# Performance work log

Measured on AMD Instinct MI355X. Metric: run time of the kernel, lower is better.

Reference implementation:

```python
import jax, jax.numpy as jnp
import numpy as np

B, S, E = 2, 2048, 2048
H, G = 16, 4
HD = E // H  # 128 head dim


def setup_inputs() -> dict:
    key = jax.random.key(0)
    k1, k2, k3, k4 = jax.random.split(key, 4)
    x = jax.random.normal(k1, (B, S, E), dtype=jnp.float32)
    mask = jnp.zeros((B, 1, S, S), dtype=jnp.float32)
    # torch nn.Linear weights stored as [in, out] for x @ W
    W1 = jax.random.normal(k2, (E, 2 * G * HD), dtype=jnp.float32) * 0.02
    W2 = jax.random.normal(k3, (E, E), dtype=jnp.float32) * 0.02
    W3 = jax.random.normal(k4, (E, E), dtype=jnp.float32) * 0.02
    return {"x": x, "mask": mask, "W1": W1, "W2": W2, "W3": W3}


def reference(x, mask, W1, W2, W3):
    b, s, e_model = x.shape
    hd = e_model // H
    # linear_1 -> rearrange 'b s (n g e) -> n b g s e'
    kv = (x @ W1).reshape(b, s, 2, G, hd).transpose(2, 0, 3, 1, 4)
    k, v = kv[0], kv[1]  # [b, g, s, e]
    # linear_2 -> 'b t (h e) -> b h t e'
    q = (x @ W2).reshape(b, s, H, hd).transpose(0, 2, 1, 3)  # [b, h, t, e]
    # NOTE: g is summed out here, exactly as in the source einsum (no sqrt scaling)
    score = jnp.einsum('bhte,bgse->bhts', q, k)
    score = jax.nn.softmax(score + mask, axis=-1)
    out = jnp.einsum('bhts,bgse->bthe', score, v)  # g summed again
    out = out.reshape(b, s, e_model)
    return out @ W3
```

## Files before the change

### kernel.cpp

```cpp
#include <hip/hip_runtime.h>
#include <cstdint>

#define S_LEN 2048
#define EMB   2048
#define NHEAD 16
#define HDIM  128
#define NFUSE 2304
#define LOG2E 1.4426950408889634f

typedef __attribute__((ext_vector_type(8))) _Float16 h8;
typedef __attribute__((ext_vector_type(4))) _Float16 h4;
typedef __attribute__((ext_vector_type(8))) short short8;
typedef __attribute__((ext_vector_type(4))) short short4v;
typedef __attribute__((ext_vector_type(4))) float f32x4;
typedef unsigned int u32;

__device__ inline short f2bf(float x) {
  union { float f; uint32_t u; } v; v.f = x;
  uint32_t r = v.u + 0x7fffu + ((v.u >> 16) & 1u);
  return (short)(r >> 16);
}
__device__ inline float bf2f(short b) {
  union { uint32_t u; float f; } v; v.u = ((uint32_t)(uint16_t)b) << 16;
  return v.f;
}
__device__ inline float fexp2(float x) {
  float r;
  __asm__ volatile("v_exp_f32 %0, %1" : "=v"(r) : "v"(x));
  return r;
}
__device__ inline u32 pkrtz(float a, float b) {
  u32 r;
  __asm__ volatile("v_cvt_pkrtz_f16_f32 %0, %1, %2" : "=v"(r) : "v"(a), "v"(b));
  return r;
}
__device__ inline void glds16(const void* g, void* l) {
  __builtin_amdgcn_global_load_lds(
      (const __attribute__((address_space(1))) u32*)g,
      (__attribute__((address_space(3))) u32*)l, 16, 0, 0);
}

__global__ __launch_bounds__(256) void reduce_w1_kernel(
    const float* __restrict__ W1, float* __restrict__ Wkv) {
  int idx = blockIdx.x * 256 + threadIdx.x;
  int i = idx >> 8;
  int c = idx & 255;
  int base = (c < 128) ? c : (c + 384);
  const float* r = W1 + (size_t)i * 1024 + base;
  Wkv[idx] = (r[0] + r[128]) + (r[256] + r[384]);
}

__global__ __launch_bounds__(256) void cvt_x_kernel(
    const float* __restrict__ src, _Float16* __restrict__ dst) {
  size_t idx = (size_t)blockIdx.x * 256 + threadIdx.x;
  float4 v = *(const float4*)(src + idx * 4);
  h4 o;
  o[0] = (_Float16)v.x; o[1] = (_Float16)v.y;
  o[2] = (_Float16)v.z; o[3] = (_Float16)v.w;
  *(h4*)(dst + idx * 4) = o;
}

__global__ __launch_bounds__(256) void cvt_mask_kernel(
    const float* __restrict__ src, short* __restrict__ dst) {
  size_t idx = (size_t)blockIdx.x * 256 + threadIdx.x;
  float4 v = *(const float4*)(src + idx * 4);
  short4v o;
  o[0] = f2bf(v.x * LOG2E); o[1] = f2bf(v.y * LOG2E);
  o[2] = f2bf(v.z * LOG2E); o[3] = f2bf(v.w * LOG2E);
  *(short4v*)(dst + idx * 4) = o;
}

__global__ __launch_bounds__(256) void transpose_f16_kernel(
    const float* __restrict__ W, _Float16* __restrict__ T, int K, int N) {
  __shared__ float Tt[64][65];
  const int tid = threadIdx.x;
  const int k0 = blockIdx.y * 64, n0 = blockIdx.x * 64;
  {
    int r = tid >> 2, c0 = (tid & 3) * 16;
    const float* src = W + (size_t)(k0 + r) * N + n0 + c0;
#pragma unroll
    for (int j = 0; j < 4; ++j) {
      float4 v = *(const float4*)(src + 4 * j);
      Tt[r][c0 + 4 * j + 0] = v.x; Tt[r][c0 + 4 * j + 1] = v.y;
      Tt[r][c0 + 4 * j + 2] = v.z; Tt[r][c0 + 4 * j + 3] = v.w;
    }
  }
  __syncthreads();
  {
    int n = tid >> 2, kc = (tid & 3) * 16;
    h8 o0, o1;
#pragma unroll
    for (int i = 0; i < 8; ++i) {
      o0[i] = (_Float16)Tt[kc + i][n];
      o1[i] = (_Float16)Tt[kc + 8 + i][n];
    }
    size_t off = (size_t)(n0 + n) * K + k0 + kc;
    *(h8*)(T + off) = o0;
    *(h8*)(T + off + 8) = o1;
  }
}

template <bool QSCALE>
__global__ __launch_bounds__(256, 3) void gemm_f16(
    const _Float16* __restrict__ A, const _Float16* __restrict__ Bt,
    float* __restrict__ C, _Float16* __restrict__ Cf,
    int M, int N, int K, int qlim) {
  extern __shared__ char smraw[];
  _Float16* sm = (_Float16*)smraw;
  const int BUFS = 8192;

  const int tid  = threadIdx.x;
  const int w    = tid >> 6;
  const int lane = tid & 63;
  const int quad = lane >> 4, col16 = lane & 15;
  const int row0 = blockIdx.y * 128, col0 = blockIdx.x * 128;
  const float esc = (col0 < qlim) ? LOG2E : 1.0f;

  const int srow  = w * 32 + (lane >> 2);
  const int kpart = (lane & 3) * 8;
  const _Float16* pA0 = A + (size_t)(row0 + srow) * K + kpart;
  const _Float16* pA1 = pA0 + (size_t)16 * K;
  const _Float16* pB0 = Bt + (size_t)(col0 + srow) * K + kpart;
  const _Float16* pB1 = pB0 + (size_t)16 * K;

  const int oA0 = (w * 32) * 32, oA1 = (w * 32 + 16) * 32;
  const int oB0 = 4096 + (w * 32) * 32, oB1 = 4096 + (w * 32 + 16) * 32;

#define STAGE_GEMM(bo)                                                        \
  do {                                                                        \
    glds16(pA0, sm + (bo) + oA0); glds16(pA1, sm + (bo) + oA1);               \
    glds16(pB0, sm + (bo) + oB0); glds16(pB1, sm + (bo) + oB1);               \
    pA0 += 32; pA1 += 32; pB0 += 32; pB1 += 32;                               \
  } while (0)

  f32x4 acc[2][8];
#pragma unroll
  for (int mt = 0; mt < 2; ++mt)
#pragma unroll
    for (int nt = 0; nt < 8; ++nt) {
      acc[mt][nt][0] = 0.f; acc[mt][nt][1] = 0.f;
      acc[mt][nt][2] = 0.f; acc[mt][nt][3] = 0.f;
    }

  const int nchunk = K >> 5;
  int bo = 0;
  STAGE_GEMM(0);

#pragma unroll 1
  for (int c = 0; c < nchunk; ++c) {
    if (c + 1 < nchunk) {
      STAGE_GEMM(bo ^ BUFS);
      __asm__ volatile("s_waitcnt vmcnt(4)" ::: "memory");
    } else {
      __asm__ volatile("s_waitcnt vmcnt(0)" ::: "memory");
    }
    __builtin_amdgcn_s_barrier();

    const _Float16* AS = sm + bo;
    const _Float16* BS = sm + bo + 4096;

    h8 af[2];
#pragma unroll
    for (int mt = 0; mt < 2; ++mt)
      af[mt] = *(const h8*)&AS[(w * 32 + mt * 16 + col16) * 32 + quad * 8];
#pragma unroll
    for (int nt = 0; nt < 8; ++nt) {
      h8 b8 = *(const h8*)&BS[(nt * 16 + col16) * 32 + quad * 8];
#pragma unroll
      for (int mt = 0; mt < 2; ++mt)
        acc[mt][nt] = __builtin_amdgcn_mfma_f32_16x16x32_f16(af[mt], b8, acc[mt][nt], 0, 0, 0);
    }
    __builtin_amdgcn_s_barrier();
    bo ^= BUFS;
  }
#undef STAGE_GEMM

#pragma unroll
  for (int mt = 0; mt < 2; ++mt)
#pragma unroll
    for (int nt = 0; nt < 8; ++nt)
#pragma unroll
      for (int r = 0; r < 4; ++r) {
        int row = row0 + w * 32 + mt * 16 + quad * 4 + r;
        int col = col0 + nt * 16 + col16;
        float v = acc[mt][nt][r];
        if constexpr (QSCALE) {
          Cf[(size_t)row * N + col] = (_Float16)(v * esc);
        } else {
          C[(size_t)row * N + col] = v;
        }
      }
}

__global__ __launch_bounds__(256) void build_vt(
    const short* __restrict__ QKh, short* __restrict__ VT) {
  __shared__ short T[64][136];
  const int tid = threadIdx.x;
  const int gs = blockIdx.x * 64;
  const int b = gs >> 11;
  const int s = gs & 2047;
  {
    int r = tid >> 2, c0 = (tid & 3) * 32;
    const short* src = QKh + (size_t)(gs + r) * NFUSE + 2176 + c0;
#pragma unroll
    for (int j = 0; j < 4; ++j)
      *(short8*)&T[r][c0 + 8 * j] = *(const short8*)(src + 8 * j);
  }
  __syncthreads();
  {
    int d = tid >> 1, c = (tid & 1) * 32;
    short* dst = VT + (size_t)(b * HDIM + d) * S_LEN + s + c;
#pragma unroll
    for (int jo = 0; jo < 4; ++jo) {
      short8 o;
#pragma unroll
      for (int i = 0; i < 8; ++i) o[i] = T[c + jo * 8 + i][d];
      *(short8*)(dst + jo * 8) = o;
    }
  }
}

__global__ __launch_bounds__(256, 2) void flash_f16(
    const _Float16* __restrict__ QKf, const _Float16* __restrict__ VT,
    const short* __restrict__ maskb, _Float16* __restrict__ AO) {
  __shared__ _Float16 KS[64 * 128];
  __shared__ _Float16 VtS[128 * 64];
  __shared__ _Float16 PsS[2 * 4 * 16 * 64];

  const int tid   = threadIdx.x;
  const int w     = tid >> 6;
  const int lane  = tid & 63;
  const int quad  = lane >> 4;
  const int col16 = lane & 15;
  const int xq    = col16 & 7;
  const int bh = blockIdx.y, b = bh >> 4, h = bh & 15;
  const int t0 = blockIdx.x * 128;

  const int jr = lane >> 4;
  const int kg = lane & 15;
  const int vr = lane >> 3;
  const int vg = lane & 7;

  _Float16* myK = KS + w * 2048;
  _Float16* myV = VtS + w * 2048;

  h8 qf[2][4];
#pragma unroll
  for (int t = 0; t < 2; ++t) {
#pragma unroll
    for (int j = 0; j < 4; ++j) {
      int rl = 4 * j + jr;
      int gq = kg ^ (rl & 7);
      size_t go = (size_t)(b * S_LEN + t0 + 64 * t + 16 * w + rl) * NFUSE
                + h * HDIM + gq * 8;
      glds16(QKf + go, myK + j * 512);
    }
    __asm__ volatile("s_waitcnt vmcnt(0)" ::: "memory");
#pragma unroll
    for (int c = 0; c < 4; ++c)
      qf[t][c] = *(const h8*)&myK[col16 * 128 + (((c * 4 + quad) ^ xq) * 8)];
    __asm__ volatile("s_waitcnt lgkmcnt(0)" ::: "memory");
  }

  const _Float16* Kbase = QKf + (size_t)b * S_LEN * NFUSE + 2048;
  const _Float16* Vbase = VT + (size_t)b * HDIM * S_LEN;
  u32 offK[4], offV[4];
#pragma unroll
  for (int j = 0; j < 4; ++j) {
    int rl = 4 * j + jr;
    offK[j] = (u32)(16 * w + rl) * NFUSE + (u32)((kg ^ (rl & 7)) * 8);
    int dl = 32 * w + 8 * j + vr;
    offV[j] = (u32)dl * S_LEN + (u32)((vg ^ (vr & 7)) * 8);
  }
  const short* pM[2];
#pragma unroll
  for (int t = 0; t < 2; ++t)
    pM[t] = maskb + (size_t)b * S_LEN * S_LEN
          + (size_t)(t0 + 64 * t + 16 * w + col16) * S_LEN + quad * 4;

#pragma unroll
  for (int j = 0; j < 4; ++j) glds16(Kbase + offK[j], myK + j * 512);
#pragma unroll
  for (int j = 0; j < 4; ++j) glds16(Vbase + offV[j], myV + j * 512);
#pragma unroll
  for (int j = 0; j < 4; ++j) { offK[j] += 64 * NFUSE; offV[j] += 64; }

  f32x4 oacc[2][8];
#pragma unroll
  for (int t = 0; t < 2; ++t)
#pragma unroll
    for (int d = 0; d < 8; ++d) {
      oacc[t][d][0] = 0.f; oacc[t][d][1] = 0.f;
      oacc[t][d][2] = 0.f; oacc[t][d][3] = 0.f;
    }
  float mrow[2] = {-3.0e38f, -3.0e38f};
  float lrow[2] = {0.f, 0.f};

#pragma unroll 1
  for (int it = 0; it < S_LEN / 64; ++it) {
    __asm__ volatile("s_waitcnt vmcnt(4)" ::: "memory");
    __builtin_amdgcn_s_barrier();

    short4v msk[2][4];
#pragma unroll
    for (int t = 0; t < 2; ++t)
#pragma unroll
      for (int nt = 0; nt < 4; ++nt)
        msk[t][nt] = *(const short4v*)(pM[t] + nt * 16);

    f32x4 sacc[2][4];
#pragma unroll
    for (int t = 0; t < 2; ++t)
#pragma unroll
      for (int nt = 0; nt < 4; ++nt) {
        sacc[t][nt][0] = 0.f; sacc[t][nt][1] = 0.f;
        sacc[t][nt][2] = 0.f; sacc[t][nt][3] = 0.f;
      }
    __builtin_amdgcn_s_setprio(1);
#pragma unroll
    for (int c = 0; c < 4; ++c)
#pragma unroll
      for (int nt = 0; nt < 4; ++nt) {
        h8 k8 = *(const h8*)&KS[(nt * 16 + col16) * 128 + (((c * 4 + quad) ^ xq) * 8)];
#pragma unroll
        for (int t = 0; t < 2; ++t)
          sacc[t][nt] = __builtin_amdgcn_mfma_f32_16x16x32_f16(k8, qf[t][c], sacc[t][nt], 0, 0, 0);
      }
    __builtin_amdgcn_s_setprio(0);

    __asm__ volatile("s_waitcnt lgkmcnt(0)" ::: "memory");
    __builtin_amdgcn_s_barrier();
    if (it + 1 < S_LEN / 64) {
#pragma unroll
      for (int j = 0; j < 4; ++j) glds16(Kbase + offK[j], myK + j * 512);
#pragma unroll
      for (int j = 0; j < 4; ++j) offK[j] += 64 * NFUSE;
    }

    if (it + 1 < S_LEN / 64) {
      __asm__ volatile("s_waitcnt vmcnt(4)" ::: "memory");
    } else {
      __asm__ volatile("s_waitcnt vmcnt(0)" ::: "memory");
    }

#pragma unroll
    for (int t = 0; t < 2; ++t) {
      float vv[4][4];
#pragma unroll
      for (int nt = 0; nt < 4; ++nt)
#pragma unroll
        for (int r = 0; r < 4; ++r)
          vv[nt][r] = sacc[t][nt][r] + bf2f(msk[t][nt][r]);
      float mx = vv[0][0];
#pragma unroll
      for (int nt = 0; nt < 4; ++nt)
#pragma unroll
        for (int r = 0; r < 4; ++r) mx = fmaxf(mx, vv[nt][r]);
      mx = fmaxf(mx, __shfl_xor(mx, 16));
      mx = fmaxf(mx, __shfl_xor(mx, 32));

      float nm = fmaxf(mrow[t], mx);
      if (__all(mx - mrow[t] <= 8.0f)) {
        nm = mrow[t];
      } else {
        float al = fexp2(mrow[t] - nm);
        lrow[t] *= al;
#pragma unroll
        for (int d = 0; d < 8; ++d) {
          oacc[t][d][0] *= al; oacc[t][d][1] *= al;
          oacc[t][d][2] *= al; oacc[t][d][3] *= al;
        }
        mrow[t] = nm;
      }

      float ps = 0.f;
      u32 pk0[4], pk1[4];
#pragma unroll
      for (int nt = 0; nt < 4; ++nt) {
        float p0 = fexp2(vv[nt][0] - nm);
        float p1 = fexp2(vv[nt][1] - nm);
        float p2 = fexp2(vv[nt][2] - nm);
        float p3 = fexp2(vv[nt][3] - nm);
        ps += (p0 + p1) + (p2 + p3);
        pk0[nt] = pkrtz(p0, p1);
        pk1[nt] = pkrtz(p2, p3);
      }
      ps += __shfl_xor(ps, 16);
      ps += __shfl_xor(ps, 32);
      lrow[t] += ps;

      int pbase = ((t * 4 + w) * 16 + col16) * 64 + (quad & 1) * 4;
#pragma unroll
      for (int nt = 0; nt < 4; ++nt) {
        uint2 pv2; pv2.x = pk0[nt]; pv2.y = pk1[nt];
        *(uint2*)&PsS[pbase + (((2 * nt + (quad >> 1)) ^ xq) * 8)] = pv2;
      }
    }

    __asm__ volatile("s_waitcnt lgkmcnt(0)" ::: "memory");
    h8 pa[2][2];
#pragma unroll
    for (int t = 0; t < 2; ++t) {
      int pb = ((t * 4 + w) * 16 + col16) * 64;
      pa[t][0] = *(const h8*)&PsS[pb + ((quad ^ xq) * 8)];
      pa[t][1] = *(const h8*)&PsS[pb + (((4 + quad) ^ xq) * 8)];
    }
    __builtin_amdgcn_s_setprio(1);
#pragma unroll
    for (int d = 0; d < 8; ++d) {
      int vo = (d * 16 + col16) * 64;
      h8 vb0 = *(const h8*)&VtS[vo + ((quad ^ xq) * 8)];
      h8 vb1 = *(const h8*)&VtS[vo + (((4 + quad) ^ xq) * 8)];
#pragma unroll
      for (int t = 0; t < 2; ++t) {
        oacc[t][d] = __builtin_amdgcn_mfma_f32_16x16x32_f16(vb0, pa[t][0], oacc[t][d], 0, 0, 0);
        oacc[t][d] = __builtin_amdgcn_mfma_f32_16x16x32_f16(vb1, pa[t][1], oacc[t][d], 0, 0, 0);
      }
    }
    __builtin_amdgcn_s_setprio(0);

    __asm__ volatile("s_waitcnt lgkmcnt(0)" ::: "memory");
    __builtin_amdgcn_s_barrier();
    if (it + 1 < S_LEN / 64) {
#pragma unroll
      for (int j = 0; j < 4; ++j) glds16(Vbase + offV[j], myV + j * 512);
#pragma unroll
      for (int j = 0; j < 4; ++j) offV[j] += 64;
    }
#pragma unroll
    for (int t = 0; t < 2; ++t) pM[t] += 64;
  }

#pragma unroll
  for (int t = 0; t < 2; ++t) {
    float inv = 1.0f / lrow[t];
    int q = t0 + 64 * t + 16 * w + col16;
    _Float16* dst = AO + (size_t)(b * S_LEN + q) * EMB + h * HDIM + quad * 4;
#pragma unroll
    for (int d = 0; d < 8; ++d) {
      h4 o4;
#pragma unroll
      for (int r = 0; r < 4; ++r) o4[r] = (_Float16)(oacc[t][d][r] * inv);
      *(h4*)(dst + d * 16) = o4;
    }
  }
}

extern "C" void kernel_launch(void* const* d_in, const int* in_sizes, int n_in,
                              void* d_out, int out_size, void* d_ws, size_t ws_size,
                              hipStream_t stream) {
  const float* x    = (const float*)d_in[0];
  const float* mask = (const float*)d_in[1];
  const float* W1   = (const float*)d_in[2];
  const float* W2   = (const float*)d_in[3];
  const float* W3   = (const float*)d_in[4];
  float* out = (float*)d_out;

  char* ws = (char*)d_ws;
  size_t off = 0;
  _Float16* xf   = (_Float16*)(ws + off); off += (size_t)4096 * 2048 * 2;
  _Float16* Wtf  = (_Float16*)(ws + off); off += (size_t)NFUSE * 2048 * 2;
  _Float16* QKf  = (_Float16*)(ws + off); off += (size_t)4096 * NFUSE * 2;
  _Float16* VT   = (_Float16*)(ws + off); off += (size_t)2 * 128 * 2048 * 2;
  _Float16* AOf  = (_Float16*)(ws + off); off += (size_t)4096 * 2048 * 2;
  float*    Wkv  = (float*)(ws + off);    off += (size_t)2048 * 256 * 4;
  short*    maskb= (short*)(ws + off);    off += (size_t)2 * 2048 * 2048 * 2;
  _Float16* W3t  = xf;

  reduce_w1_kernel<<<2048, 256, 0, stream>>>(W1, Wkv);
  cvt_x_kernel<<<8192, 256, 0, stream>>>(x, xf);
  cvt_mask_kernel<<<8192, 256, 0, stream>>>(mask, maskb);
  transpose_f16_kernel<<<dim3(32, 32), 256, 0, stream>>>(W2, Wtf, 2048, 2048);
  transpose_f16_kernel<<<dim3(4, 32), 256, 0, stream>>>(
      Wkv, Wtf + (size_t)2048 * 2048, 2048, 256);

  gemm_f16<true><<<dim3(NFUSE / 128, 32), 256, 32768, stream>>>(
      xf, Wtf, nullptr, QKf, 4096, NFUSE, 2048, 2048);

  build_vt<<<64, 256, 0, stream>>>((const short*)QKf, (short*)VT);

  flash_f16<<<dim3(S_LEN / 128, 2 * NHEAD), 256, 0, stream>>>(
      QKf, VT, maskb, AOf);

  transpose_f16_kernel<<<dim3(32, 32), 256, 0, stream>>>(W3, W3t, 2048, 2048);
  gemm_f16<false><<<dim3(16, 32), 256, 32768, stream>>>(
      AOf, W3t, out, nullptr, 4096, 2048, 2048, 0);
}
```

Measured before the change: 370.2 us.

## Halve flash query tile to 64 rows and stage mask tiles via LDS async loads

The flash attention kernel now processes 64 query rows per block instead of 128, which doubles the grid and halves per-thread accumulator registers. The mask is no longer read with direct global loads each iteration. It is prefetched into LDS with async global-to-LDS copies alongside K, and the wait counts are adjusted to match. This trades twice the K/V traffic per query and lower K/V reuse for higher occupancy and latency hiding, and takes mask loads off the critical path.

```diff
diff --git a/kernel.cpp b/kernel.cpp
--- a/kernel.cpp
+++ b/kernel.cpp
@@ -225,7 +225,8 @@
     const short* __restrict__ maskb, _Float16* __restrict__ AO) {
   __shared__ _Float16 KS[64 * 128];
   __shared__ _Float16 VtS[128 * 64];
-  __shared__ _Float16 PsS[2 * 4 * 16 * 64];
+  __shared__ _Float16 PsS[4 * 16 * 64];
+  __shared__ short    MkS[4 * 16 * 64];
 
   const int tid   = threadIdx.x;
   const int w     = tid >> 6;
@@ -234,7 +235,7 @@
   const int col16 = lane & 15;
   const int xq    = col16 & 7;
   const int bh = blockIdx.y, b = bh >> 4, h = bh & 15;
-  const int t0 = blockIdx.x * 128;
+  const int t0 = blockIdx.x * 64;
 
   const int jr = lane >> 4;
   const int kg = lane & 15;
@@ -243,28 +244,30 @@
 
   _Float16* myK = KS + w * 2048;
   _Float16* myV = VtS + w * 2048;
-
-  h8 qf[2][4];
-#pragma unroll
-  for (int t = 0; t < 2; ++t) {
+  short*    myM = MkS + w * 1024;
+  _Float16* myP = PsS + w * 1024;
+
+  h8 qf[4];
+  {
 #pragma unroll
     for (int j = 0; j < 4; ++j) {
       int rl = 4 * j + jr;
       int gq = kg ^ (rl & 7);
-      size_t go = (size_t)(b * S_LEN + t0 + 64 * t + 16 * w + rl) * NFUSE
+      size_t go = (size_t)(b * S_LEN + t0 + 16 * w + rl) * NFUSE
                 + h * HDIM + gq * 8;
       glds16(QKf + go, myK + j * 512);
     }
     __asm__ volatile("s_waitcnt vmcnt(0)" ::: "memory");
 #pragma unroll
     for (int c = 0; c < 4; ++c)
-      qf[t][c] = *(const h8*)&myK[col16 * 128 + (((c * 4 + quad) ^ xq) * 8)];
+      qf[c] = *(const h8*)&myK[col16 * 128 + (((c * 4 + quad) ^ xq) * 8)];
     __asm__ volatile("s_waitcnt lgkmcnt(0)" ::: "memory");
   }
 
   const _Float16* Kbase = QKf + (size_t)b * S_LEN * NFUSE + 2048;
   const _Float16* Vbase = VT + (size_t)b * HDIM * S_LEN;
-  u32 offK[4], offV[4];
+  const short*    Mbase = maskb + (size_t)b * S_LEN * S_LEN;
+  u32 offK[4], offV[4], offM[2];
 #pragma unroll
   for (int j = 0; j < 4; ++j) {
     int rl = 4 * j + jr;
@@ -272,59 +275,56 @@
     int dl = 32 * w + 8 * j + vr;
     offV[j] = (u32)dl * S_LEN + (u32)((vg ^ (vr & 7)) * 8);
   }
-  const short* pM[2];
-#pragma unroll
-  for (int t = 0; t < 2; ++t)
-    pM[t] = maskb + (size_t)b * S_LEN * S_LEN
-          + (size_t)(t0 + 64 * t + 16 * w + col16) * S_LEN + quad * 4;
+#pragma unroll
+  for (int j = 0; j < 2; ++j) {
+    int mrw = j * 8 + vr;
+    int mq  = t0 + 16 * w + mrw;
+    offM[j] = (u32)mq * S_LEN + (u32)((vg ^ (mrw & 7)) * 8);
+  }
 
 #pragma unroll
   for (int j = 0; j < 4; ++j) glds16(Kbase + offK[j], myK + j * 512);
 #pragma unroll
+  for (int j = 0; j < 2; ++j) glds16(Mbase + offM[j], myM + j * 512);
+#pragma unroll
   for (int j = 0; j < 4; ++j) glds16(Vbase + offV[j], myV + j * 512);
 #pragma unroll
   for (int j = 0; j < 4; ++j) { offK[j] += 64 * NFUSE; offV[j] += 64; }
-
-  f32x4 oacc[2][8];
-#pragma unroll
-  for (int t = 0; t < 2; ++t)
-#pragma unroll
-    for (int d = 0; d < 8; ++d) {
-      oacc[t][d][0] = 0.f; oacc[t][d][1] = 0.f;
-      oacc[t][d][2] = 0.f; oacc[t][d][3] = 0.f;
-    }
-  float mrow[2] = {-3.0e38f, -3.0e38f};
-  float lrow[2] = {0.f, 0.f};
+#pragma unroll
+  for (int j = 0; j < 2; ++j) offM[j] += 64;
+
+  f32x4 oacc[8];
+#pragma unroll
+  for (int d = 0; d < 8; ++d) {
+    oacc[d][0] = 0.f; oacc[d][1] = 0.f;
+    oacc[d][2] = 0.f; oacc[d][3] = 0.f;
+  }
+  float mrow = -3.0e38f, lrow = 0.f;
 
 #pragma unroll 1
   for (int it = 0; it < S_LEN / 64; ++it) {
     __asm__ volatile("s_waitcnt vmcnt(4)" ::: "memory");
     __builtin_amdgcn_s_barrier();
 
-    short4v msk[2][4];
-#pragma unroll
-    for (int t = 0; t < 2; ++t)
-#pragma unroll
-      for (int nt = 0; nt < 4; ++nt)
-        msk[t][nt] = *(const short4v*)(pM[t] + nt * 16);
-
-    f32x4 sacc[2][4];
-#pragma unroll
-    for (int t = 0; t < 2; ++t)
-#pragma unroll
-      for (int nt = 0; nt < 4; ++nt) {
-        sacc[t][nt][0] = 0.f; sacc[t][nt][1] = 0.f;
-        sacc[t][nt][2] = 0.f; sacc[t][nt][3] = 0.f;
-      }
+    short4v msk[4];
+#pragma unroll
+    for (int nt = 0; nt < 4; ++nt)
+      msk[nt] = *(const short4v*)
+          &myM[col16 * 64 + (((quad + nt * 4) ^ (xq << 1)) << 2)];
+
+    f32x4 sacc[4];
+#pragma unroll
+    for (int nt = 0; nt < 4; ++nt) {
+      sacc[nt][0] = 0.f; sacc[nt][1] = 0.f;
+      sacc[nt][2] = 0.f; sacc[nt][3] = 0.f;
+    }
     __builtin_amdgcn_s_setprio(1);
 #pragma unroll
     for (int c = 0; c < 4; ++c)
 #pragma unroll
       for (int nt = 0; nt < 4; ++nt) {
         h8 k8 = *(const h8*)&KS[(nt * 16 + col16) * 128 + (((c * 4 + quad) ^ xq) * 8)];
-#pragma unroll
-        for (int t = 0; t < 2; ++t)
-          sacc[t][nt] = __builtin_amdgcn_mfma_f32_16x16x32_f16(k8, qf[t][c], sacc[t][nt], 0, 0, 0);
+        sacc[nt] = __builtin_amdgcn_mfma_f32_16x16x32_f16(k8, qf[c], sacc[nt], 0, 0, 0);
       }
     __builtin_amdgcn_s_setprio(0);
 
@@ -334,23 +334,26 @@
 #pragma unroll
       for (int j = 0; j < 4; ++j) glds16(Kbase + offK[j], myK + j * 512);
 #pragma unroll
+      for (int j = 0; j < 2; ++j) glds16(Mbase + offM[j], myM + j * 512);
+#pragma unroll
       for (int j = 0; j < 4; ++j) offK[j] += 64 * NFUSE;
+#pragma unroll
+      for (int j = 0; j < 2; ++j) offM[j] += 64;
     }
 
     if (it + 1 < S_LEN / 64) {
-      __asm__ volatile("s_waitcnt vmcnt(4)" ::: "memory");
+      __asm__ volatile("s_waitcnt vmcnt(6)" ::: "memory");
     } else {
       __asm__ volatile("s_waitcnt vmcnt(0)" ::: "memory");
     }
 
-#pragma unroll
-    for (int t = 0; t < 2; ++t) {
+    {
       float vv[4][4];
 #pragma unroll
       for (int nt = 0; nt < 4; ++nt)
 #pragma unroll
         for (int r = 0; r < 4; ++r)
-          vv[nt][r] = sacc[t][nt][r] + bf2f(msk[t][nt][r]);
+          vv[nt][r] = sacc[nt][r] + bf2f(msk[nt][r]);
       float mx = vv[0][0];
 #pragma unroll
       for (int nt = 0; nt < 4; ++nt)
@@ -359,18 +362,18 @@
       mx = fmaxf(mx, __shfl_xor(mx, 16));
       mx = fmaxf(mx, __shfl_xor(mx, 32));
 
-      float nm = fmaxf(mrow[t], mx);
-      if (__all(mx - mrow[t] <= 8.0f)) {
-        nm = mrow[t];
+      float nm = fmaxf(mrow, mx);
+      if (__all(mx - mrow <= 8.0f)) {
+        nm = mrow;
       } else {
-        float al = fexp2(mrow[t] - nm);
-        lrow[t] *= al;
+        float al = fexp2(mrow - nm);
+        lrow *= al;
 #pragma unroll
         for (int d = 0; d < 8; ++d) {
-          oacc[t][d][0] *= al; oacc[t][d][1] *= al;
-          oacc[t][d][2] *= al; oacc[t][d][3] *= al;
+          oacc[d][0] *= al; oacc[d][1] *= al;
+          oacc[d][2] *= al; oacc[d][3] *= al;
         }
-        mrow[t] = nm;
+        mrow = nm;
       }
 
       float ps = 0.f;
@@ -387,35 +390,27 @@
       }
       ps += __shfl_xor(ps, 16);
       ps += __shfl_xor(ps, 32);
-      lrow[t] += ps;
-
-      int pbase = ((t * 4 + w) * 16 + col16) * 64 + (quad & 1) * 4;
+      lrow += ps;
+
+      int pbase = col16 * 64 + (quad & 1) * 4;
 #pragma unroll
       for (int nt = 0; nt < 4; ++nt) {
         uint2 pv2; pv2.x = pk0[nt]; pv2.y = pk1[nt];
-        *(uint2*)&PsS[pbase + (((2 * nt + (quad >> 1)) ^ xq) * 8)] = pv2;
+        *(uint2*)&myP[pbase + (((2 * nt + (quad >> 1)) ^ xq) * 8)] = pv2;
       }
     }
 
     __asm__ volatile("s_waitcnt lgkmcnt(0)" ::: "memory");
-    h8 pa[2][2];
-#pragma unroll
-    for (int t = 0; t < 2; ++t) {
-      int pb = ((t * 4 + w) * 16 + col16) * 64;
-      pa[t][0] = *(const h8*)&PsS[pb + ((quad ^ xq) * 8)];
-      pa[t][1] = *(const h8*)&PsS[pb + (((4 + quad) ^ xq) * 8)];
-    }
+    h8 pa0 = *(const h8*)&myP[col16 * 64 + ((quad ^ xq) * 8)];
+    h8 pa1 = *(const h8*)&myP[col16 * 64 + (((4 + quad) ^ xq) * 8)];
     __builtin_amdgcn_s_setprio(1);
 #pragma unroll
     for (int d = 0; d < 8; ++d) {
       int vo = (d * 16 + col16) * 64;
       h8 vb0 = *(const h8*)&VtS[vo + ((quad ^ xq) * 8)];
       h8 vb1 = *(const h8*)&VtS[vo + (((4 + quad) ^ xq) * 8)];
-#pragma unroll
-      for (int t = 0; t < 2; ++t) {
-        oacc[t][d] = __builtin_amdgcn_mfma_f32_16x16x32_f16(vb0, pa[t][0], oacc[t][d], 0, 0, 0);
-        oacc[t][d] = __builtin_amdgcn_mfma_f32_16x16x32_f16(vb1, pa[t][1], oacc[t][d], 0, 0, 0);
-      }
+      oacc[d] = __builtin_amdgcn_mfma_f32_16x16x32_f16(vb0, pa0, oacc[d], 0, 0, 0);
+      oacc[d] = __builtin_amdgcn_mfma_f32_16x16x32_f16(vb1, pa1, oacc[d], 0, 0, 0);
     }
     __builtin_amdgcn_s_setprio(0);
 
@@ -427,20 +422,17 @@
 #pragma unroll
       for (int j = 0; j < 4; ++j) offV[j] += 64;
     }
-#pragma unroll
-    for (int t = 0; t < 2; ++t) pM[t] += 64;
-  }
-
-#pragma unroll
-  for (int t = 0; t < 2; ++t) {
-    float inv = 1.0f / lrow[t];
-    int q = t0 + 64 * t + 16 * w + col16;
+  }
+
+  {
+    float inv = 1.0f / lrow;
+    int q = t0 + 16 * w + col16;
     _Float16* dst = AO + (size_t)(b * S_LEN + q) * EMB + h * HDIM + quad * 4;
 #pragma unroll
     for (int d = 0; d < 8; ++d) {
       h4 o4;
 #pragma unroll
-      for (int r = 0; r < 4; ++r) o4[r] = (_Float16)(oacc[t][d][r] * inv);
+      for (int r = 0; r < 4; ++r) o4[r] = (_Float16)(oacc[d][r] * inv);
       *(h4*)(dst + d * 16) = o4;
     }
   }
@@ -479,7 +471,7 @@
 
   build_vt<<<64, 256, 0, stream>>>((const short*)QKf, (short*)VT);
 
-  flash_f16<<<dim3(S_LEN / 128, 2 * NHEAD), 256, 0, stream>>>(
+  flash_f16<<<dim3(S_LEN / 64, 2 * NHEAD), 256, 0, stream>>>(
       QKf, VT, maskb, AOf);
 
   transpose_f16_kernel<<<dim3(32, 32), 256, 0, stream>>>(W3, W3t, 2048, 2048);
```

After: 390.3 us. 5.4% more time.
